# Performance work log

Measured on AMD Instinct MI355X. Metric: run time of the kernel, lower is better.

Reference implementation:

```python
import jax, jax.numpy as jnp
import numpy as np

EMBED_DIM = 1024


def setup_inputs() -> dict:
    key = jax.random.key(0)
    ks = jax.random.split(key, 8)
    B, S, D = 4, 2048, EMBED_DIM
    scale = 1.0 / np.sqrt(D)
    x = jax.random.normal(ks[0], (B, S, D), dtype=jnp.float32)
    mask = jnp.zeros((S, S), dtype=jnp.float32)
    # nn.Linear default init ~ U(-1/sqrt(fan_in), 1/sqrt(fan_in)); exact dist irrelevant for correctness
    w_q = jax.random.uniform(ks[1], (D, D), jnp.float32, -scale, scale)
    b_q = jax.random.uniform(ks[2], (D,), jnp.float32, -scale, scale)
    w_k = jax.random.uniform(ks[3], (D, D), jnp.float32, -scale, scale)
    b_k = jax.random.uniform(ks[4], (D,), jnp.float32, -scale, scale)
    w_v = jax.random.uniform(ks[5], (D, D), jnp.float32, -scale, scale)
    b_v = jax.random.uniform(ks[6], (D,), jnp.float32, -scale, scale)
    return {"x": x, "mask": mask, "w_q": w_q, "b_q": b_q,
            "w_k": w_k, "b_k": b_k, "w_v": w_v, "b_v": b_v}


def reference(x, mask, w_q, b_q, w_k, b_k, w_v, b_v):
    D = x.shape[-1]
    # nn.Linear computes x @ W^T + b
    Q = jnp.einsum('bsd,ed->bse', x, w_q) + b_q
    K = jnp.einsum('bsd,ed->bse', x, w_k) + b_k
    V = jnp.einsum('bsd,ed->bse', x, w_v) + b_v
    scores = jnp.einsum('bqd,bkd->bqk', Q, K) / jnp.sqrt(jnp.asarray(D, x.dtype))
    scores = scores + mask  # additive mask, broadcast over batch
    attn = jax.nn.softmax(scores, axis=-1)
    return jnp.einsum('bqk,bkd->bqd', attn, V)
```

## Files before the change

### kernel.cpp

```cpp
#include <hip/hip_runtime.h>


typedef __attribute__((ext_vector_type(8))) short short8;
typedef __attribute__((ext_vector_type(4))) short short4v;
typedef __attribute__((ext_vector_type(4))) float float4v;

__device__ __forceinline__ short f2bf(float f) {
  unsigned u = __builtin_bit_cast(unsigned, f);
  u += 0x7fffu + ((u >> 16) & 1u);
  return (short)(u >> 16);
}
__device__ __forceinline__ float bf2f(short s) {
  unsigned u = ((unsigned)(unsigned short)s) << 16;
  return __builtin_bit_cast(float, u);
}

__device__ __forceinline__ void gl2lds16(const void* g, void* l) {
  __builtin_amdgcn_global_load_lds((const __attribute__((address_space(1))) void*)g,
                                   (__attribute__((address_space(3))) void*)l, 16, 0, 0);
}

__global__ __launch_bounds__(256) void prep_kernel(const float* __restrict__ x,
                                                   const float* __restrict__ wq,
                                                   const float* __restrict__ wk,
                                                   const float* __restrict__ wv,
                                                   const float* __restrict__ bq,
                                                   const float* __restrict__ bk,
                                                   short* __restrict__ x_bf,
                                                   short* __restrict__ w_bf,
                                                   float* __restrict__ bcat) {
  int b = blockIdx.x;
  if (b < 3072) {
    int seg = b >> 10;
    const float* w = seg == 0 ? wq : (seg == 1 ? wk : wv);
    int i = (b - (seg << 10)) * 256 + threadIdx.x;
    float4v v = ((const float4v*)w)[i];
    short4v o;
    o.x = f2bf(v.x); o.y = f2bf(v.y); o.z = f2bf(v.z); o.w = f2bf(v.w);
    ((short4v*)(w_bf + (long)seg * 1048576))[i] = o;
  } else if (b < 11264) {
    int i = (b - 3072) * 256 + threadIdx.x;
    float4v v = ((const float4v*)x)[i];
    short4v o;
    o.x = f2bf(v.x); o.y = f2bf(v.y); o.z = f2bf(v.z); o.w = f2bf(v.w);
    ((short4v*)x_bf)[i] = o;
  } else {
    int i = (b - 11264) * 256 + threadIdx.x;
    if (i < 2048) bcat[i] = i < 1024 ? bq[i] : bk[i - 1024];
  }
}

template <int EPI>
__device__ __forceinline__ void gemm_body(const short* __restrict__ A,
                                          const short* __restrict__ Bm,
                                          void* __restrict__ C,
                                          const float* __restrict__ aux,
                                          float* __restrict__ rsum, float scale,
                                          int N, int Kd, int Bld, int m0, int n0,
                                          short (*As)[64], short (*Bs)[64]) {
  const int t = threadIdx.x;
  const int lane = t & 63, wave = t >> 6;
  const int wm = (wave & 1) * 64, wn = (wave >> 1) * 64;
  const int col = lane & 15, quad = lane >> 4;

  const int r_loc = lane >> 3, slot = lane & 7;
  const int cch = slot ^ r_loc;
  const int sw = col & 7;

  float4v acc[4][4] = {};

  for (int kt = 0; kt < Kd; kt += 64) {
#pragma unroll
    for (int u = 0; u < 4; ++u) {
      const int rowbase = wave * 32 + u * 8;
      gl2lds16(&A[(long)(m0 + rowbase + r_loc) * Kd + kt + cch * 8],
               &As[rowbase][0] + lane * 8);
      gl2lds16(&Bm[(long)(n0 + rowbase + r_loc) * Bld + kt + cch * 8],
               &Bs[rowbase][0] + lane * 8);
    }
    __syncthreads();

#pragma unroll
    for (int s = 0; s < 2; ++s) {
      short8 af[4], bfr[4];
#pragma unroll
      for (int i = 0; i < 4; ++i)
        af[i] = *(const short8*)&As[wm + i * 16 + col][((s * 4 + quad) ^ sw) * 8];
#pragma unroll
      for (int j = 0; j < 4; ++j)
        bfr[j] = *(const short8*)&Bs[wn + j * 16 + col][((s * 4 + quad) ^ sw) * 8];
#pragma unroll
      for (int i = 0; i < 4; ++i)
#pragma unroll
        for (int j = 0; j < 4; ++j)
          acc[i][j] = __builtin_amdgcn_mfma_f32_16x16x32_bf16(af[i], bfr[j], acc[i][j], 0, 0, 0);
    }
    __syncthreads();
  }

  float* invb = (float*)Bs;
  if (EPI == 2) {
    if (t < 128) {
      float s = 0.f;
#pragma unroll
      for (int p = 0; p < 32; ++p) s += aux[p * 8192 + m0 + t];
      invb[t] = __builtin_amdgcn_rcpf(s);
    }
    __syncthreads();
  }

  const float LOG2E = 1.44269504f;
  const float c1 = scale * LOG2E;
#pragma unroll
  for (int i = 0; i < 4; ++i) {
    float invv[4], addm[4], rsum4[4] = {0.f, 0.f, 0.f, 0.f};
    if (EPI == 2) {
#pragma unroll
      for (int r = 0; r < 4; ++r) invv[r] = invb[wm + i * 16 + quad * 4 + r];
    }
    if (EPI == 3) {
#pragma unroll
      for (int r = 0; r < 4; ++r) addm[r] = aux[m0 + wm + i * 16 + quad * 4 + r];
    }
#pragma unroll
    for (int j = 0; j < 4; ++j) {
      const int n = n0 + wn + j * 16 + col;
      float addn = 0.f;
      if (EPI == 0) addn = aux[n];
#pragma unroll
      for (int r = 0; r < 4; ++r) {
        const int m = m0 + wm + i * 16 + quad * 4 + r;
        float v = acc[i][j][r];
        if (EPI == 0) {
          ((short*)C)[(long)m * N + n] = f2bf(v + addn);
        } else if (EPI == 1) {
          float mv = aux[(long)m * N + n];
          float e = exp2f(fmaf(v, c1, mv * LOG2E));
          short q = f2bf(e);
          ((short*)C)[(long)m * N + n] = q;
          rsum4[r] += bf2f(q);
        } else if (EPI == 2) {
          ((float*)C)[(long)m * N + n] = v * invv[r];
        } else {
          ((short*)C)[(long)m * N + n] = f2bf(v + addm[r]);
        }
      }
    }
    if (EPI == 1) {
#pragma unroll
      for (int r = 0; r < 4; ++r) {
        float s = rsum4[r];
        s += __shfl_xor(s, 1);
        s += __shfl_xor(s, 2);
        s += __shfl_xor(s, 4);
        s += __shfl_xor(s, 8);
        if (col == 0)
          rsum[(wn >> 6) * 8192 + m0 + wm + i * 16 + quad * 4 + r] = s;
      }
    }
  }
}

__global__ __launch_bounds__(256) void qkv_kernel(const short* __restrict__ x_bf,
                                                  const short* __restrict__ w_bf,
                                                  short* __restrict__ QK,
                                                  short* __restrict__ Vt,
                                                  const float* __restrict__ bcat,
                                                  const float* __restrict__ bv) {
  __shared__ alignas(16) short As[128][64];
  __shared__ alignas(16) short Bs[128][64];
  const int b = blockIdx.x;
  if (b < 1024) {
    const int g = (b & 7) * 128 + (b >> 3);
    const int bz = g >> 9, rr = g & 511;
    const int m0 = (rr >> 3) * 128, n0 = (rr & 7) * 128;
    gemm_body<0>(x_bf, w_bf + (long)bz * 1048576, QK + (long)bz * 8388608,
                 bcat + bz * 1024, nullptr, 1.f, 1024, 1024, 1024, m0, n0, As, Bs);
  } else {
    const int v = b - 1024;
    const int g = (v & 7) * 64 + (v >> 3);
    const int m0 = (g >> 6) * 128, n0 = (g & 63) * 128;
    gemm_body<3>(w_bf + 2097152, x_bf, Vt, bv, nullptr, 1.f,
                 8192, 1024, 1024, m0, n0, As, Bs);
  }
}

__global__ __launch_bounds__(256) void scores_kernel(const short* __restrict__ Q,
                                                     const short* __restrict__ Kb,
                                                     short* __restrict__ P,
                                                     const float* __restrict__ mask,
                                                     float* __restrict__ rspart) {
  __shared__ alignas(16) short As[128][64];
  __shared__ alignas(16) short Bs[128][64];
  const int id = blockIdx.x;
  const int g = (id & 7) * 128 + (id >> 3);
  const int bz = g >> 8, t2 = g & 255;
  const int m0 = (t2 >> 4) * 128, n0 = (t2 & 15) * 128;
  gemm_body<1>(Q + (long)bz * 2097152, Kb + (long)bz * 2097152,
               P + (long)bz * 4194304, mask,
               rspart + (n0 >> 7) * 2 * 8192 + bz * 2048, 0.03125f,
               2048, 1024, 1024, m0, n0, As, Bs);
}

__global__ __launch_bounds__(256) void pv_kernel(const short* __restrict__ P,
                                                 const short* __restrict__ Vt,
                                                 float* __restrict__ out,
                                                 const float* __restrict__ rspart) {
  __shared__ alignas(16) short As[128][64];
  __shared__ alignas(16) short Bs[128][64];
  const int id = blockIdx.x;
  const int g = (id & 7) * 64 + (id >> 3);
  const int bz = g >> 7, t2 = g & 127;
  const int m0 = (t2 >> 3) * 128, n0 = (t2 & 7) * 128;
  gemm_body<2>(P + (long)bz * 4194304, Vt + (long)bz * 2048,
               out + (long)bz * 2097152, rspart + bz * 2048, nullptr, 1.f,
               1024, 2048, 8192, m0, n0, As, Bs);
}

extern "C" void kernel_launch(void* const* d_in, const int* in_sizes, int n_in,
                              void* d_out, int out_size, void* d_ws, size_t ws_size,
                              hipStream_t stream) {
  const float* x    = (const float*)d_in[0];
  const float* mask = (const float*)d_in[1];
  const float* wq   = (const float*)d_in[2];
  const float* bq   = (const float*)d_in[3];
  const float* wk   = (const float*)d_in[4];
  const float* bk   = (const float*)d_in[5];
  const float* wv   = (const float*)d_in[6];
  const float* bv   = (const float*)d_in[7];
  float* out = (float*)d_out;

  char* ws = (char*)d_ws;
  const size_t MB = 1024 * 1024;
  short* x_bf   = (short*)(ws);
  float* rspart = (float*)(ws);
  short* w_bf   = (short*)(ws + 16 * MB);
  short* QK     = (short*)(ws + 22 * MB);
  short* Vt     = (short*)(ws + 54 * MB);
  short* P      = (short*)(ws + 70 * MB);
  float* bcat   = (float*)(ws + 70 * MB);

  prep_kernel<<<11272, 256, 0, stream>>>(x, wq, wk, wv, bq, bk, x_bf, w_bf, bcat);

  qkv_kernel<<<1536, 256, 0, stream>>>(x_bf, w_bf, QK, Vt, bcat, bv);

  short* Q  = QK;
  short* Kb = QK + 8388608;

  scores_kernel<<<1024, 256, 0, stream>>>(Q, Kb, P, mask, rspart);

  pv_kernel<<<512, 256, 0, stream>>>(P, Vt, out, rspart);
}
```

Measured before the change: 272.1 us.

## Switch GEMMs to 256x256 tiles with 8 waves and double-buffered LDS pipeline

The shared GEMM body moves from 128x128 tiles with 4 waves to 256x256 tiles with 8 waves. It double-buffers LDS, issuing global-to-LDS loads for the next K-steps in quarter-sized pieces interleaved with four MFMA phases, using s_setprio and explicit vmcnt waits. Grids shrink accordingly and the row-sum partial indexing is adapted to 4 column-waves per 256 tile. This is meant to hide load latency and raise data reuse per tile. In exchange it leaves fewer blocks (128 for pv on 256 CUs), uses 128KB of LDS per block, and puts heavy register pressure on the 8x4 accumulator array.

```diff
diff --git a/kernel.cpp b/kernel.cpp
--- a/kernel.cpp
+++ b/kernel.cpp
@@ -50,6 +50,15 @@
   }
 }
 
+__device__ __forceinline__ void stage_half(const short* __restrict__ g, int ld,
+                                           int grow0, int kt, short* lds, int t) {
+  const int r = t >> 3;
+  const int cch = (t & 7) ^ (r & 7);
+  const long co = (long)kt + cch * 8;
+  gl2lds16(g + (long)(grow0 + r) * ld + co, lds + t * 8);
+  gl2lds16(g + (long)(grow0 + 64 + r) * ld + co, lds + 4096 + t * 8);
+}
+
 template <int EPI>
 __device__ __forceinline__ void gemm_body(const short* __restrict__ A,
                                           const short* __restrict__ Bm,
@@ -59,48 +68,115 @@
                                           int N, int Kd, int Bld, int m0, int n0,
                                           short (*As)[64], short (*Bs)[64]) {
   const int t = threadIdx.x;
-  const int lane = t & 63, wave = t >> 6;
-  const int wm = (wave & 1) * 64, wn = (wave >> 1) * 64;
+  const int lane = t & 63;
+  const int wave = t >> 6;
+  const int wm = (wave >> 2) * 128;
+  const int wn = (wave & 3) * 64;
   const int col = lane & 15, quad = lane >> 4;
-
-  const int r_loc = lane >> 3, slot = lane & 7;
-  const int cch = slot ^ r_loc;
   const int sw = col & 7;
-
-  float4v acc[4][4] = {};
-
-  for (int kt = 0; kt < Kd; kt += 64) {
-#pragma unroll
-    for (int u = 0; u < 4; ++u) {
-      const int rowbase = wave * 32 + u * 8;
-      gl2lds16(&A[(long)(m0 + rowbase + r_loc) * Kd + kt + cch * 8],
-               &As[rowbase][0] + lane * 8);
-      gl2lds16(&Bm[(long)(n0 + rowbase + r_loc) * Bld + kt + cch * 8],
-               &Bs[rowbase][0] + lane * 8);
-    }
-    __syncthreads();
-
-#pragma unroll
-    for (int s = 0; s < 2; ++s) {
-      short8 af[4], bfr[4];
-#pragma unroll
-      for (int i = 0; i < 4; ++i)
-        af[i] = *(const short8*)&As[wm + i * 16 + col][((s * 4 + quad) ^ sw) * 8];
-#pragma unroll
-      for (int j = 0; j < 4; ++j)
-        bfr[j] = *(const short8*)&Bs[wn + j * 16 + col][((s * 4 + quad) ^ sw) * 8];
-#pragma unroll
-      for (int i = 0; i < 4; ++i)
-#pragma unroll
-        for (int j = 0; j < 4; ++j)
-          acc[i][j] = __builtin_amdgcn_mfma_f32_16x16x32_bf16(af[i], bfr[j], acc[i][j], 0, 0, 0);
-    }
-    __syncthreads();
-  }
-
-  float* invb = (float*)Bs;
+  const int NT = Kd >> 6;
+
+  float4v acc[8][4] = {};
+
+  stage_half(A, Kd, m0, 0, &As[0][0], t);
+  stage_half(A, Kd, m0 + 128, 0, &As[128][0], t);
+  stage_half(Bm, Bld, n0, 0, &Bs[0][0], t);
+  stage_half(Bm, Bld, n0 + 128, 0, &Bs[128][0], t);
+  if (NT > 1) {
+    stage_half(Bm, Bld, n0, 64, &Bs[256][0], t);
+    stage_half(Bm, Bld, n0 + 128, 64, &Bs[384][0], t);
+    asm volatile("s_waitcnt vmcnt(4)" ::: "memory");
+  } else {
+    asm volatile("s_waitcnt vmcnt(0)" ::: "memory");
+  }
+  __builtin_amdgcn_s_barrier();
+
+#pragma unroll 2
+  for (int k = 0; k < NT; ++k) {
+    const int buf = (k & 1) << 8;
+    const int nbf = 256 - buf;
+    short8 a[4][2], b0[2][2], b1[2][2];
+
+#pragma unroll
+    for (int i = 0; i < 4; ++i)
+#pragma unroll
+      for (int s = 0; s < 2; ++s)
+        a[i][s] = *(const short8*)&As[buf + wm + i * 16 + col][(((s * 4 + quad) ^ sw)) * 8];
+#pragma unroll
+    for (int j = 0; j < 2; ++j)
+#pragma unroll
+      for (int s = 0; s < 2; ++s)
+        b0[j][s] = *(const short8*)&Bs[buf + wn + j * 16 + col][(((s * 4 + quad) ^ sw)) * 8];
+    if (k + 1 < NT) stage_half(A, Kd, m0, (k + 1) * 64, &As[nbf][0], t);
+    __builtin_amdgcn_s_barrier();
+    __builtin_amdgcn_s_setprio(1);
+#pragma unroll
+    for (int i = 0; i < 4; ++i)
+#pragma unroll
+      for (int j = 0; j < 2; ++j)
+#pragma unroll
+        for (int s = 0; s < 2; ++s)
+          acc[i][j] = __builtin_amdgcn_mfma_f32_16x16x32_bf16(a[i][s], b0[j][s], acc[i][j], 0, 0, 0);
+    __builtin_amdgcn_s_setprio(0);
+    __builtin_amdgcn_s_barrier();
+
+#pragma unroll
+    for (int j = 0; j < 2; ++j)
+#pragma unroll
+      for (int s = 0; s < 2; ++s)
+        b1[j][s] = *(const short8*)&Bs[buf + wn + (j + 2) * 16 + col][(((s * 4 + quad) ^ sw)) * 8];
+    if (k + 1 < NT) stage_half(A, Kd, m0 + 128, (k + 1) * 64, &As[nbf + 128][0], t);
+    __builtin_amdgcn_s_barrier();
+    __builtin_amdgcn_s_setprio(1);
+#pragma unroll
+    for (int i = 0; i < 4; ++i)
+#pragma unroll
+      for (int j = 0; j < 2; ++j)
+#pragma unroll
+        for (int s = 0; s < 2; ++s)
+          acc[i][j + 2] = __builtin_amdgcn_mfma_f32_16x16x32_bf16(a[i][s], b1[j][s], acc[i][j + 2], 0, 0, 0);
+    __builtin_amdgcn_s_setprio(0);
+    __builtin_amdgcn_s_barrier();
+
+#pragma unroll
+    for (int i = 0; i < 4; ++i)
+#pragma unroll
+      for (int s = 0; s < 2; ++s)
+        a[i][s] = *(const short8*)&As[buf + wm + (i + 4) * 16 + col][(((s * 4 + quad) ^ sw)) * 8];
+    if (k + 2 < NT) stage_half(Bm, Bld, n0, (k + 2) * 64, &Bs[buf][0], t);
+    __builtin_amdgcn_s_barrier();
+    __builtin_amdgcn_s_setprio(1);
+#pragma unroll
+    for (int i = 0; i < 4; ++i)
+#pragma unroll
+      for (int j = 0; j < 2; ++j)
+#pragma unroll
+        for (int s = 0; s < 2; ++s)
+          acc[i + 4][j + 2] = __builtin_amdgcn_mfma_f32_16x16x32_bf16(a[i][s], b1[j][s], acc[i + 4][j + 2], 0, 0, 0);
+    __builtin_amdgcn_s_setprio(0);
+    __builtin_amdgcn_s_barrier();
+
+    if (k + 2 < NT) stage_half(Bm, Bld, n0 + 128, (k + 2) * 64, &Bs[buf + 128][0], t);
+    __builtin_amdgcn_s_barrier();
+    __builtin_amdgcn_s_setprio(1);
+#pragma unroll
+    for (int i = 0; i < 4; ++i)
+#pragma unroll
+      for (int j = 0; j < 2; ++j)
+#pragma unroll
+        for (int s = 0; s < 2; ++s)
+          acc[i + 4][j] = __builtin_amdgcn_mfma_f32_16x16x32_bf16(a[i][s], b0[j][s], acc[i + 4][j], 0, 0, 0);
+    __builtin_amdgcn_s_setprio(0);
+    if (k + 1 < NT) {
+      if (k + 2 < NT) asm volatile("s_waitcnt vmcnt(4)" ::: "memory");
+      else            asm volatile("s_waitcnt vmcnt(0)" ::: "memory");
+    }
+    __builtin_amdgcn_s_barrier();
+  }
+
+  float* invb = (float*)&Bs[0][0];
   if (EPI == 2) {
-    if (t < 128) {
+    if (t < 256) {
       float s = 0.f;
 #pragma unroll
       for (int p = 0; p < 32; ++p) s += aux[p * 8192 + m0 + t];
@@ -112,7 +188,7 @@
   const float LOG2E = 1.44269504f;
   const float c1 = scale * LOG2E;
 #pragma unroll
-  for (int i = 0; i < 4; ++i) {
+  for (int i = 0; i < 8; ++i) {
     float invv[4], addm[4], rsum4[4] = {0.f, 0.f, 0.f, 0.f};
     if (EPI == 2) {
 #pragma unroll
@@ -155,63 +231,62 @@
         s += __shfl_xor(s, 4);
         s += __shfl_xor(s, 8);
         if (col == 0)
-          rsum[(wn >> 6) * 8192 + m0 + wm + i * 16 + quad * 4 + r] = s;
+          rsum[(wave & 3) * 8192 + m0 + wm + i * 16 + quad * 4 + r] = s;
       }
     }
   }
 }
 
-__global__ __launch_bounds__(256) void qkv_kernel(const short* __restrict__ x_bf,
-                                                  const short* __restrict__ w_bf,
-                                                  short* __restrict__ QK,
-                                                  short* __restrict__ Vt,
-                                                  const float* __restrict__ bcat,
-                                                  const float* __restrict__ bv) {
-  __shared__ alignas(16) short As[128][64];
-  __shared__ alignas(16) short Bs[128][64];
+__global__ __launch_bounds__(512, 2) void qkv_kernel(const short* __restrict__ x_bf,
+                                                     const short* __restrict__ w_bf,
+                                                     short* __restrict__ QK,
+                                                     short* __restrict__ Vt,
+                                                     const float* __restrict__ bcat,
+                                                     const float* __restrict__ bv) {
+  __shared__ alignas(16) short As[512][64];
+  __shared__ alignas(16) short Bs[512][64];
   const int b = blockIdx.x;
-  if (b < 1024) {
-    const int g = (b & 7) * 128 + (b >> 3);
-    const int bz = g >> 9, rr = g & 511;
-    const int m0 = (rr >> 3) * 128, n0 = (rr & 7) * 128;
+  const int g = (b & 7) * 48 + (b >> 3);
+  if (g < 256) {
+    const int bz = g >> 7, r = g & 127;
+    const int m0 = (r >> 2) * 256, n0 = (r & 3) * 256;
     gemm_body<0>(x_bf, w_bf + (long)bz * 1048576, QK + (long)bz * 8388608,
                  bcat + bz * 1024, nullptr, 1.f, 1024, 1024, 1024, m0, n0, As, Bs);
   } else {
-    const int v = b - 1024;
-    const int g = (v & 7) * 64 + (v >> 3);
-    const int m0 = (g >> 6) * 128, n0 = (g & 63) * 128;
+    const int v = g - 256;
+    const int m0 = (v >> 5) * 256, n0 = (v & 31) * 256;
     gemm_body<3>(w_bf + 2097152, x_bf, Vt, bv, nullptr, 1.f,
                  8192, 1024, 1024, m0, n0, As, Bs);
   }
 }
 
-__global__ __launch_bounds__(256) void scores_kernel(const short* __restrict__ Q,
-                                                     const short* __restrict__ Kb,
-                                                     short* __restrict__ P,
-                                                     const float* __restrict__ mask,
-                                                     float* __restrict__ rspart) {
-  __shared__ alignas(16) short As[128][64];
-  __shared__ alignas(16) short Bs[128][64];
-  const int id = blockIdx.x;
-  const int g = (id & 7) * 128 + (id >> 3);
-  const int bz = g >> 8, t2 = g & 255;
-  const int m0 = (t2 >> 4) * 128, n0 = (t2 & 15) * 128;
+__global__ __launch_bounds__(512, 2) void scores_kernel(const short* __restrict__ Q,
+                                                        const short* __restrict__ Kb,
+                                                        short* __restrict__ P,
+                                                        const float* __restrict__ mask,
+                                                        float* __restrict__ rspart) {
+  __shared__ alignas(16) short As[512][64];
+  __shared__ alignas(16) short Bs[512][64];
+  const int b = blockIdx.x;
+  const int g = (b & 7) * 32 + (b >> 3);
+  const int bz = g >> 6, t2 = g & 63;
+  const int m0 = (t2 >> 3) * 256, n0 = (t2 & 7) * 256;
   gemm_body<1>(Q + (long)bz * 2097152, Kb + (long)bz * 2097152,
                P + (long)bz * 4194304, mask,
-               rspart + (n0 >> 7) * 2 * 8192 + bz * 2048, 0.03125f,
+               rspart + (long)(n0 >> 8) * 4 * 8192 + bz * 2048, 0.03125f,
                2048, 1024, 1024, m0, n0, As, Bs);
 }
 
-__global__ __launch_bounds__(256) void pv_kernel(const short* __restrict__ P,
-                                                 const short* __restrict__ Vt,
-                                                 float* __restrict__ out,
-                                                 const float* __restrict__ rspart) {
-  __shared__ alignas(16) short As[128][64];
-  __shared__ alignas(16) short Bs[128][64];
-  const int id = blockIdx.x;
-  const int g = (id & 7) * 64 + (id >> 3);
-  const int bz = g >> 7, t2 = g & 127;
-  const int m0 = (t2 >> 3) * 128, n0 = (t2 & 7) * 128;
+__global__ __launch_bounds__(512, 2) void pv_kernel(const short* __restrict__ P,
+                                                    const short* __restrict__ Vt,
+                                                    float* __restrict__ out,
+                                                    const float* __restrict__ rspart) {
+  __shared__ alignas(16) short As[512][64];
+  __shared__ alignas(16) short Bs[512][64];
+  const int b = blockIdx.x;
+  const int g = (b & 7) * 16 + (b >> 3);
+  const int bz = g >> 5, t2 = g & 31;
+  const int m0 = (t2 >> 2) * 256, n0 = (t2 & 3) * 256;
   gemm_body<2>(P + (long)bz * 4194304, Vt + (long)bz * 2048,
                out + (long)bz * 2097152, rspart + bz * 2048, nullptr, 1.f,
                1024, 2048, 8192, m0, n0, As, Bs);
@@ -242,12 +317,12 @@
 
   prep_kernel<<<11272, 256, 0, stream>>>(x, wq, wk, wv, bq, bk, x_bf, w_bf, bcat);
 
-  qkv_kernel<<<1536, 256, 0, stream>>>(x_bf, w_bf, QK, Vt, bcat, bv);
+  qkv_kernel<<<384, 512, 0, stream>>>(x_bf, w_bf, QK, Vt, bcat, bv);
 
   short* Q  = QK;
   short* Kb = QK + 8388608;
 
-  scores_kernel<<<1024, 256, 0, stream>>>(Q, Kb, P, mask, rspart);
-
-  pv_kernel<<<512, 256, 0, stream>>>(P, Vt, out, rspart);
-}
+  scores_kernel<<<256, 512, 0, stream>>>(Q, Kb, P, mask, rspart);
+
+  pv_kernel<<<128, 512, 0, stream>>>(P, Vt, out, rspart);
+}
```

After: 275.9 us. About the same (+1.4%).
